# Kernel tuning notes

Hardware: AMD Instinct MI355X
Metric: run time of the kernel (lower is better)

## Reference

```python
import jax, jax.numpy as jnp
import numpy as np

N, E, D, H, L = 10000, 80000, 1024, 8, 2
C = D // H          # 128 per-head channels
NEG = 0.2           # GATv2 default negative_slope


def setup_inputs() -> dict:
    k = jax.random.split(jax.random.key(0), 16)
    s = 0.02
    return {
        "x": jax.random.normal(k[0], (N, D), jnp.float32),
        "edge_index": jax.random.randint(k[1], (2, E), 0, N),
        "edge_attr": jax.random.randint(k[2], (E,), 0, 3),
        "node_types": jax.random.randint(k[3], (N,), 0, 5),
        "node_type_emb": s * jax.random.normal(k[4], (5, D), jnp.float32),
        "edge_type_emb": s * jax.random.normal(k[5], (3, D), jnp.float32),
        "Wl": s * jax.random.normal(k[6], (L, D, D), jnp.float32),
        "bl": jnp.zeros((L, D), jnp.float32),
        "Wr": s * jax.random.normal(k[7], (L, D, D), jnp.float32),
        "br": jnp.zeros((L, D), jnp.float32),
        "We": s * jax.random.normal(k[8], (L, D, D), jnp.float32),
        "att": s * jax.random.normal(k[9], (L, H, C), jnp.float32),
        "conv_bias": jnp.zeros((L, D), jnp.float32),
        "out_W": s * jax.random.normal(k[10], (D, D), jnp.float32),
        "out_b": jnp.zeros((D,), jnp.float32),
    }


def _gatv2(h, src, dst, ee, Wl, bl, Wr, br, We, att, b):
    """PyG GATv2Conv: concat=True, add_self_loops=True (fill_value='mean')."""
    n = h.shape[0]
    xl = (h @ Wl + bl).reshape(n, H, C)   # source transform (lin_l)
    xr = (h @ Wr + br).reshape(n, H, C)   # target transform (lin_r)
    # self loops: edge_attr of a loop = mean of raw incoming edge feats
    cnt = jax.ops.segment_sum(jnp.ones(src.shape, jnp.float32), dst, num_segments=n)
    loop_attr = jax.ops.segment_sum(ee, dst, num_segments=n) / jnp.maximum(cnt, 1.0)[:, None]
    loops = jnp.arange(n)
    s2 = jnp.concatenate([src, loops])
    d2 = jnp.concatenate([dst, loops])
    ea = jnp.concatenate([ee, loop_attr], axis=0)          # [E+N, D]
    ep = (ea @ We).reshape(-1, H, C)                        # lin_edge (no bias)
    e = jax.nn.leaky_relu(xl[s2] + xr[d2] + ep, NEG)        # [E+N, H, C]
    logit = jnp.einsum('ehc,hc->eh', e, att)                # attention logits
    # segment softmax over destination nodes (every node has a self loop)
    m = jax.ops.segment_max(logit, d2, num_segments=n)
    a = jnp.exp(logit - m[d2])
    alpha = a / jax.ops.segment_sum(a, d2, num_segments=n)[d2]
    out = jax.ops.segment_sum(alpha[:, :, None] * xl[s2], d2, num_segments=n)
    return out.reshape(n, D) + b


def reference(x, edge_index, edge_attr, node_types, node_type_emb, edge_type_emb,
              Wl, bl, Wr, br, We, att, conv_bias, out_W, out_b):
    h = x + node_type_emb[node_types]
    ee = edge_type_emb[edge_attr]
    src, dst = edge_index[0], edge_index[1]
    for i in range(L):  # num_layers = 2
        h = h + jax.nn.relu(_gatv2(h, src, dst, ee, Wl[i], bl[i], Wr[i], br[i],
                                   We[i], att[i], conv_bias[i]))
    return h @ out_W + out_b
```

## Files before the change

### kernel.cpp

```cpp
#include <hip/hip_runtime.h>
#include <hip/hip_bf16.h>
#include <stdint.h>

typedef __bf16 bf16_t;
typedef bf16_t bf16x8 __attribute__((ext_vector_type(8)));
typedef bf16_t bf16x4 __attribute__((ext_vector_type(4)));
typedef float f32x4 __attribute__((ext_vector_type(4)));

#define NN 10000
#define EE 80000
#define DD 1024
#define LL 2
#define MPAD 10112
#define NEGS 0.2f

#define GLOAD_LDS16(g, l) \
    __builtin_amdgcn_global_load_lds((__attribute__((address_space(1))) void*)(void*)(g), \
                                     (__attribute__((address_space(3))) void*)(l), 16, 0, 0)

__global__ __launch_bounds__(256)
void preamble(const float* __restrict__ Wl, const float* __restrict__ Wr,
              const float* __restrict__ outW, bf16_t* __restrict__ WT,
              bf16_t* __restrict__ OWT,
              const float* __restrict__ x, const int* __restrict__ ntypes,
              const float* __restrict__ nte, bf16_t* __restrict__ hbuf,
              const float* __restrict__ bl, const float* __restrict__ br,
              const float* __restrict__ outb, float* __restrict__ biasb,
              float* __restrict__ M3L, int* __restrict__ deg3)
{
    __shared__ float tile[64][65];
    int b = blockIdx.x;
    int tid = threadIdx.x;
    if (b < 1280) {
        int z = b >> 8, rem = b & 255;
        int bx = rem & 15, by = rem >> 4;
        const float* src;
        bf16_t* dstp;
        switch (z) {
            case 0: src = Wl;                       dstp = WT;                        break;
            case 1: src = Wr;                       dstp = WT + (size_t)1024*1024;    break;
            case 2: src = Wl + (size_t)1024*1024;   dstp = WT + (size_t)2*1024*1024;  break;
            case 3: src = Wr + (size_t)1024*1024;   dstp = WT + (size_t)3*1024*1024;  break;
            default: src = outW;                    dstp = OWT;                       break;
        }
        int tx = tid & 15, ty = tid >> 4;
#pragma unroll
        for (int p = 0; p < 4; ++p) {
            int r = ty + p*16;
            f32x4 rv = *(const f32x4*)(src + (size_t)(by*64 + r)*1024 + bx*64 + tx*4);
#pragma unroll
            for (int j = 0; j < 4; ++j) tile[r][tx*4 + j] = rv[j];
        }
        __syncthreads();
        int v = tid & 7, u0 = tid >> 3;
#pragma unroll
        for (int p = 0; p < 2; ++p) {
            int u = u0 + p*32;
            bf16x8 ov;
#pragma unroll
            for (int j = 0; j < 8; ++j) ov[j] = (bf16_t)tile[v*8 + j][u];
            *(bf16x8*)(dstp + (size_t)(bx*64 + u)*1024 + by*64 + v*8) = ov;
        }
    } else if (b < 6336) {
        size_t idx = ((size_t)(b - 1280)*256 + tid) * 8;
        if (idx >= (size_t)MPAD*1024) return;
        int n = (int)(idx >> 10);
        int c = (int)(idx & 1023);
        bf16x8 outv;
        if (n < NN) {
            const float* xp = x + (size_t)n*1024 + c;
            int t = ntypes[n];
            const float* ep = nte + (size_t)t*1024 + c;
            f32x4 xa = *(const f32x4*)(xp);
            f32x4 xb = *(const f32x4*)(xp + 4);
            f32x4 ea = *(const f32x4*)(ep);
            f32x4 eb = *(const f32x4*)(ep + 4);
#pragma unroll
            for (int j = 0; j < 4; ++j) {
                outv[j]     = (bf16_t)(xa[j] + ea[j]);
                outv[4 + j] = (bf16_t)(xb[j] + eb[j]);
            }
        } else {
#pragma unroll
            for (int j = 0; j < 8; ++j) outv[j] = (bf16_t)0.f;
        }
        *(bf16x8*)(hbuf + idx) = outv;
    } else if (b < 6356) {
        int i = (b - 6336)*256 + tid;
        if (i < 4096) {
            int l = i >> 11, j = i & 2047;
            biasb[i] = (j < 1024) ? bl[l*1024 + j] : br[l*1024 + j - 1024];
        } else if (i < 5120) {
            biasb[i] = outb[i - 4096];
        }
    } else if (b < 6380) {
        int i = (b - 6356)*256 + tid;
        if (i < LL*3072) M3L[i] = 0.f;
    } else {
        int i = (b - 6380)*256 + tid;
        if (i < 3*NN) deg3[i] = 0;
    }
}

__global__ __launch_bounds__(256)
void compute_m3_all(const float* __restrict__ ete, const float* __restrict__ We,
                    float* __restrict__ M3L)
{
    int l   = blockIdx.x >> 8;
    int bid = blockIdx.x & 255;
    const float* WeL = We + (size_t)l*1024*1024;
    float* M3 = M3L + l*3072;
    int j  = (bid & 3) * 256 + threadIdx.x;
    int k0 = (bid >> 2) * 16;
    float a0 = 0.f, a1 = 0.f, a2 = 0.f;
#pragma unroll
    for (int kk = 0; kk < 16; ++kk) {
        int k = k0 + kk;
        float w = WeL[(size_t)k*1024 + j];
        a0 += ete[k]        * w;
        a1 += ete[1024 + k] * w;
        a2 += ete[2048 + k] * w;
    }
    atomicAdd(&M3[j],        a0);
    atomicAdd(&M3[1024 + j], a1);
    atomicAdd(&M3[2048 + j], a2);
}

__global__ void hist_k(const int* __restrict__ dsts, const int* __restrict__ etype,
                       int* __restrict__ deg3)
{
    int e = blockIdx.x*256 + threadIdx.x;
    if (e < EE) atomicAdd(&deg3[dsts[e]*3 + etype[e]], 1);
}

__global__ __launch_bounds__(1024)
void scan_csr(const int* __restrict__ deg3, int* __restrict__ rp3, int* __restrict__ cursor3)
{
    __shared__ int tot[1024];
    int t = threadIdx.x;
    int base = t * 30;
    int v[30];
    int run = 0;
#pragma unroll
    for (int j = 0; j < 30; ++j) {
        int i = base + j;
        int d = (i < 3*NN) ? deg3[i] : 0;
        run += d;
        v[j] = run;
    }
    tot[t] = run;
    __syncthreads();
    for (int d = 1; d < 1024; d <<= 1) {
        int xv = (t >= d) ? tot[t - d] : 0;
        __syncthreads();
        tot[t] += xv;
        __syncthreads();
    }
    int ex = (t == 0) ? 0 : tot[t - 1];
#pragma unroll
    for (int j = 0; j < 30; ++j) {
        int i = base + j;
        if (i < 3*NN) {
            int incl = ex + v[j];
            rp3[i + 1] = incl;
            if (i + 1 < 3*NN) cursor3[i + 1] = incl;
        }
    }
    if (t == 0) { rp3[0] = 0; cursor3[0] = 0; }
}

__global__ void fill_csr(const int* __restrict__ srcs, const int* __restrict__ dsts,
                         const int* __restrict__ etype, int* __restrict__ cursor3,
                         int* __restrict__ sorted_src)
{
    int e = blockIdx.x*256 + threadIdx.x;
    if (e < EE) {
        int d = dsts[e];
        int t = etype[e];
        int pos = atomicAdd(&cursor3[d*3 + t], 1);
        sorted_src[pos] = srcs[e];
    }
}

template <typename OT>
__global__ __launch_bounds__(256)
void gemm_bt(const bf16_t* __restrict__ A, const bf16_t* __restrict__ BT,
             const float* __restrict__ bias, OT* __restrict__ Cmat,
             int K, int Ntot, int storeM, int mtiles, int ntiles)
{
    __shared__ __align__(16) bf16_t As[128*64];
    __shared__ __align__(16) bf16_t Bs[128*64];
    const int tid  = threadIdx.x;
    const int wave = tid >> 6;
    const int lane = tid & 63;

    const int GROUP_M = 8;
    int pid = blockIdx.x;
    int in_group = GROUP_M * ntiles;
    int gid = pid / in_group;
    int first_m = gid * GROUP_M;
    int gsz = mtiles - first_m; if (gsz > GROUP_M) gsz = GROUP_M;
    int local = pid % in_group;
    const int m0 = (first_m + (local % gsz)) * 128;
    const int n0 = (local / gsz) * 128;

    const int wm = (wave & 1) * 64;
    const int wn = (wave >> 1) * 64;
    const int quad = lane >> 4;
    const int l16  = lane & 15;

    const int srow = lane >> 3;
    const int gcol = ((lane & 7) ^ srow) * 8;

    f32x4 acc[4][4];
    f32x4 zero = {0.f, 0.f, 0.f, 0.f};
#pragma unroll
    for (int i = 0; i < 4; ++i)
#pragma unroll
        for (int j = 0; j < 4; ++j) acc[i][j] = zero;

    const bf16_t* aBase = A  + (size_t)(m0 + wave*8 + srow) * K + gcol;
    const bf16_t* bBase = BT + (size_t)(n0 + wave*8 + srow) * K + gcol;
    bf16_t* asDst = As + wave*512;
    bf16_t* bsDst = Bs + wave*512;

    for (int k0 = 0; k0 < K; k0 += 64) {
#pragma unroll
        for (int j = 0; j < 4; ++j)
            GLOAD_LDS16(aBase + (size_t)(j*32)*K + k0, asDst + j*2048);
#pragma unroll
        for (int j = 0; j < 4; ++j)
            GLOAD_LDS16(bBase + (size_t)(j*32)*K + k0, bsDst + j*2048);
        __syncthreads();
#pragma unroll
        for (int kk = 0; kk < 2; ++kk) {
            bf16x8 af[4], bfr[4];
#pragma unroll
            for (int mi = 0; mi < 4; ++mi) {
                int row = wm + mi*16 + l16;
                int ch  = ((kk*4 + quad) ^ (row & 7)) * 8;
                af[mi] = *(const bf16x8*)(As + row*64 + ch);
            }
#pragma unroll
            for (int ni = 0; ni < 4; ++ni) {
                int row = wn + ni*16 + l16;
                int ch  = ((kk*4 + quad) ^ (row & 7)) * 8;
                bfr[ni] = *(const bf16x8*)(Bs + row*64 + ch);
            }
#pragma unroll
            for (int mi = 0; mi < 4; ++mi)
#pragma unroll
                for (int ni = 0; ni < 4; ++ni)
                    acc[mi][ni] = __builtin_amdgcn_mfma_f32_16x16x32_bf16(af[mi], bfr[ni], acc[mi][ni], 0, 0, 0);
        }
        __syncthreads();
    }

#pragma unroll
    for (int mi = 0; mi < 4; ++mi) {
#pragma unroll
        for (int ni = 0; ni < 4; ++ni) {
            int col = n0 + wn + ni*16 + l16;
            float bv = bias[col];
#pragma unroll
            for (int r = 0; r < 4; ++r) {
                int row = m0 + wm + mi*16 + quad*4 + r;
                if (row < storeM)
                    Cmat[(size_t)row * Ntot + col] = (OT)(acc[mi][ni][r] + bv);
            }
        }
    }
}

__global__ __launch_bounds__(256)
void fused_edge(const int* __restrict__ rp3, const int* __restrict__ ssrc,
                const bf16_t* __restrict__ XLXR,
                const float* __restrict__ M3, const float* __restrict__ attv,
                const float* __restrict__ cbias, bf16_t* __restrict__ hbuf)
{
    int node = blockIdx.x*2 + (threadIdx.x >> 7);
    int q = threadIdx.x & 127;
    int c8 = q * 8;

    int b   = __builtin_amdgcn_readfirstlane(rp3[3*node]);
    int t1g = __builtin_amdgcn_readfirstlane(rp3[3*node + 1]);
    int t2g = __builtin_amdgcn_readfirstlane(rp3[3*node + 2]);
    int en  = __builtin_amdgcn_readfirstlane(rp3[3*node + 3]);

    bf16x8 xlv = *(const bf16x8*)(XLXR + (size_t)node*2048 + c8);
    bf16x8 xrv = *(const bf16x8*)(XLXR + (size_t)node*2048 + 1024 + c8);
    float xr[8], at[8], q0[8], q1[8], q2[8];
#pragma unroll
    for (int j = 0; j < 8; ++j) xr[j] = (float)xrv[j];
    f32x4 a_lo = *(const f32x4*)(attv + c8);
    f32x4 a_hi = *(const f32x4*)(attv + c8 + 4);
#pragma unroll
    for (int j = 0; j < 4; ++j) { at[j] = a_lo[j]; at[4+j] = a_hi[j]; }
#pragma unroll
    for (int j = 0; j < 8; ++j) {
        q0[j] = xr[j] + M3[c8 + j];
        q1[j] = xr[j] + M3[1024 + c8 + j];
        q2[j] = xr[j] + M3[2048 + c8 + j];
    }

    float acc[8] = {0.f, 0.f, 0.f, 0.f, 0.f, 0.f, 0.f, 0.f};
    float den = 0.f;

    auto body = [&](int i, const float (&p)[8]) {
        int s = ssrc[i];
        bf16x8 xs = *(const bf16x8*)(XLXR + (size_t)s*2048 + c8);
        float x[8];
        float part = 0.f;
#pragma unroll
        for (int j = 0; j < 8; ++j) {
            x[j] = (float)xs[j];
            float v = x[j] + p[j];
            v = fmaxf(v, NEGS * v);
            part += v * at[j];
        }
        part += __shfl_xor(part, 1);
        part += __shfl_xor(part, 2);
        part += __shfl_xor(part, 4);
        part += __shfl_xor(part, 8);
        part = fminf(fmaxf(part, -60.f), 60.f);
        float pe = __expf(part);
        den += pe;
#pragma unroll
        for (int j = 0; j < 8; ++j) acc[j] += pe * x[j];
    };

#pragma unroll 2
    for (int i = b; i < t1g; ++i)   body(i, q0);
#pragma unroll 2
    for (int i = t1g; i < t2g; ++i) body(i, q1);
#pragma unroll 2
    for (int i = t2g; i < en; ++i)  body(i, q2);

    float cnt0 = (float)(t1g - b);
    float cnt1 = (float)(t2g - t1g);
    float cnt2 = (float)(en - t2g);
    float degf = cnt0 + cnt1 + cnt2;
    float inv = 1.f / fmaxf(degf, 1.f);
    float w0 = cnt0 * inv, w1 = cnt1 * inv, w2 = cnt2 * inv;
    float sw = w0 + w1 + w2;
    float sx[8];
    float sp = 0.f;
#pragma unroll
    for (int j = 0; j < 8; ++j) {
        sx[j] = (float)xlv[j];
        float u = sx[j] + xr[j]*(1.f - sw) + w0*q0[j] + w1*q1[j] + w2*q2[j];
        u = fmaxf(u, NEGS * u);
        sp += u * at[j];
    }
    sp += __shfl_xor(sp, 1);
    sp += __shfl_xor(sp, 2);
    sp += __shfl_xor(sp, 4);
    sp += __shfl_xor(sp, 8);
    sp = fminf(fmaxf(sp, -60.f), 60.f);
    float ps = __expf(sp);
    den += ps;
#pragma unroll
    for (int j = 0; j < 8; ++j) acc[j] += ps * sx[j];

    float invd = 1.f / den;
    bf16x8 hv = *(const bf16x8*)(hbuf + (size_t)node*1024 + c8);
    bf16x8 outv;
#pragma unroll
    for (int j = 0; j < 8; ++j)
        outv[j] = (bf16_t)((float)hv[j] + fmaxf(acc[j]*invd + cbias[c8 + j], 0.f));
    *(bf16x8*)(hbuf + (size_t)node*1024 + c8) = outv;
}

extern "C" void kernel_launch(void* const* d_in, const int* in_sizes, int n_in,
                              void* d_out, int out_size, void* d_ws, size_t ws_size,
                              hipStream_t stream)
{
    (void)in_sizes; (void)n_in; (void)out_size; (void)ws_size;
    const float* x     = (const float*)d_in[0];
    const int*   eidx  = (const int*)d_in[1];
    const int*   etype = (const int*)d_in[2];
    const int*   ntyp  = (const int*)d_in[3];
    const float* nte   = (const float*)d_in[4];
    const float* ete   = (const float*)d_in[5];
    const float* Wl    = (const float*)d_in[6];
    const float* bl    = (const float*)d_in[7];
    const float* Wr    = (const float*)d_in[8];
    const float* br    = (const float*)d_in[9];
    const float* We    = (const float*)d_in[10];
    const float* attw  = (const float*)d_in[11];
    const float* cbias = (const float*)d_in[12];
    const float* outW  = (const float*)d_in[13];
    const float* outb  = (const float*)d_in[14];
    const int* srcs = eidx;
    const int* dsts = eidx + EE;

    char* wsp = (char*)d_ws;
    size_t off = 0;
    auto carve = [&](size_t bytes) -> void* {
        void* pp = wsp + off;
        off += (bytes + 255) & ~(size_t)255;
        return pp;
    };
    bf16_t* hbuf  = (bf16_t*)carve((size_t)MPAD*1024*2);
    bf16_t* XLXR  = (bf16_t*)carve((size_t)MPAD*2048*2);
    bf16_t* WT    = (bf16_t*)carve((size_t)LL*2048*1024*2);
    bf16_t* OWT   = (bf16_t*)carve((size_t)1024*1024*2);
    float*  M3L   = (float*)carve((size_t)LL*3072*4);
    float*  biasb = (float*)carve(5120*4);
    int* deg3    = (int*)carve((size_t)3*NN*4);
    int* rp3     = (int*)carve((size_t)(3*NN+1)*4);
    int* cursor3 = (int*)carve((size_t)3*NN*4);
    int* ssrc    = (int*)carve((size_t)EE*4);

    preamble<<<6498, 256, 0, stream>>>(Wl, Wr, outW, WT, OWT,
                                       x, ntyp, nte, hbuf,
                                       bl, br, outb, biasb, M3L, deg3);
    compute_m3_all<<<512, 256, 0, stream>>>(ete, We, M3L);
    hist_k<<<(EE + 255)/256, 256, 0, stream>>>(dsts, etype, deg3);
    scan_csr<<<1, 1024, 0, stream>>>(deg3, rp3, cursor3);
    fill_csr<<<(EE + 255)/256, 256, 0, stream>>>(srcs, dsts, etype, cursor3, ssrc);

    for (int l = 0; l < LL; ++l) {
        gemm_bt<bf16_t><<<79*16, 256, 0, stream>>>(hbuf, WT + (size_t)l*2048*1024,
                                                   biasb + l*2048, XLXR,
                                                   1024, 2048, MPAD, 79, 16);
        fused_edge<<<NN/2, 256, 0, stream>>>(rp3, ssrc, XLXR, M3L + l*3072, attw + l*1024,
                                             cbias + l*1024, hbuf);
    }

    gemm_bt<float><<<79*8, 256, 0, stream>>>(hbuf, OWT, biasb + 4096, (float*)d_out,
                                             1024, 1024, NN, 79, 8);
}
```

Measured before the change: 406.9 us.

## Fold M3 and histogram kernels into preamble; prefetch next edge in gather loop

The separate M3 (edge-type embedding times We) and degree-histogram kernels are merged into the preamble. Each of 24 blocks there now computes a full 1024-long dot product per output with no atomics, and deg3 is zeroed with a memset beforehand. In the fused edge kernel, the three per-type loops become one loop that software-prefetches the next source row before computing the current one. This cuts launch count and aims to hide gather latency, but adds a branch per edge and leaves 24 long-running preamble blocks that may lengthen the preamble's tail.

```diff
diff --git a/kernel.cpp b/kernel.cpp
--- a/kernel.cpp
+++ b/kernel.cpp
@@ -26,7 +26,10 @@
               const float* __restrict__ nte, bf16_t* __restrict__ hbuf,
               const float* __restrict__ bl, const float* __restrict__ br,
               const float* __restrict__ outb, float* __restrict__ biasb,
-              float* __restrict__ M3L, int* __restrict__ deg3)
+              const float* __restrict__ ete, const float* __restrict__ We,
+              float* __restrict__ M3L,
+              const int* __restrict__ dsts, const int* __restrict__ etype,
+              int* __restrict__ deg3)
 {
     __shared__ float tile[64][65];
     int b = blockIdx.x;
@@ -94,43 +97,22 @@
             biasb[i] = outb[i - 4096];
         }
     } else if (b < 6380) {
-        int i = (b - 6356)*256 + tid;
-        if (i < LL*3072) M3L[i] = 0.f;
+        int idx = b - 6356;
+        int l  = idx / 12;
+        int rem = idx % 12;
+        int t  = rem >> 2;
+        int j  = (rem & 3) * 256 + tid;
+        const float* WeL = We + (size_t)l*1024*1024 + j;
+        const float* ev  = ete + t*1024;
+        float a = 0.f;
+#pragma unroll 8
+        for (int k = 0; k < 1024; ++k)
+            a += ev[k] * WeL[(size_t)k*1024];
+        M3L[l*3072 + t*1024 + j] = a;
     } else {
-        int i = (b - 6380)*256 + tid;
-        if (i < 3*NN) deg3[i] = 0;
-    }
-}
-
-__global__ __launch_bounds__(256)
-void compute_m3_all(const float* __restrict__ ete, const float* __restrict__ We,
-                    float* __restrict__ M3L)
-{
-    int l   = blockIdx.x >> 8;
-    int bid = blockIdx.x & 255;
-    const float* WeL = We + (size_t)l*1024*1024;
-    float* M3 = M3L + l*3072;
-    int j  = (bid & 3) * 256 + threadIdx.x;
-    int k0 = (bid >> 2) * 16;
-    float a0 = 0.f, a1 = 0.f, a2 = 0.f;
-#pragma unroll
-    for (int kk = 0; kk < 16; ++kk) {
-        int k = k0 + kk;
-        float w = WeL[(size_t)k*1024 + j];
-        a0 += ete[k]        * w;
-        a1 += ete[1024 + k] * w;
-        a2 += ete[2048 + k] * w;
-    }
-    atomicAdd(&M3[j],        a0);
-    atomicAdd(&M3[1024 + j], a1);
-    atomicAdd(&M3[2048 + j], a2);
-}
-
-__global__ void hist_k(const int* __restrict__ dsts, const int* __restrict__ etype,
-                       int* __restrict__ deg3)
-{
-    int e = blockIdx.x*256 + threadIdx.x;
-    if (e < EE) atomicAdd(&deg3[dsts[e]*3 + etype[e]], 1);
+        int e = (b - 6380)*256 + tid;
+        if (e < EE) atomicAdd(&deg3[dsts[e]*3 + etype[e]], 1);
+    }
 }
 
 __global__ __launch_bounds__(1024)
@@ -306,14 +288,18 @@
     float acc[8] = {0.f, 0.f, 0.f, 0.f, 0.f, 0.f, 0.f, 0.f};
     float den = 0.f;
 
-    auto body = [&](int i, const float (&p)[8]) {
-        int s = ssrc[i];
-        bf16x8 xs = *(const bf16x8*)(XLXR + (size_t)s*2048 + c8);
+    bf16x8 xs_cur, xs_next;
+    if (b < en) {
+        int s0 = ssrc[b];
+        xs_cur = *(const bf16x8*)(XLXR + (size_t)s0*2048 + c8);
+    }
+
+    auto compute = [&](const float (&p)[8]) {
         float x[8];
         float part = 0.f;
 #pragma unroll
         for (int j = 0; j < 8; ++j) {
-            x[j] = (float)xs[j];
+            x[j] = (float)xs_cur[j];
             float v = x[j] + p[j];
             v = fmaxf(v, NEGS * v);
             part += v * at[j];
@@ -329,12 +315,16 @@
         for (int j = 0; j < 8; ++j) acc[j] += pe * x[j];
     };
 
-#pragma unroll 2
-    for (int i = b; i < t1g; ++i)   body(i, q0);
-#pragma unroll 2
-    for (int i = t1g; i < t2g; ++i) body(i, q1);
-#pragma unroll 2
-    for (int i = t2g; i < en; ++i)  body(i, q2);
+    for (int i = b; i < en; ++i) {
+        if (i + 1 < en) {
+            int sn = ssrc[i + 1];
+            xs_next = *(const bf16x8*)(XLXR + (size_t)sn*2048 + c8);
+        }
+        if (i < t1g)      compute(q0);
+        else if (i < t2g) compute(q1);
+        else              compute(q2);
+        xs_cur = xs_next;
+    }
 
     float cnt0 = (float)(t1g - b);
     float cnt1 = (float)(t2g - t1g);
@@ -412,11 +402,12 @@
     int* cursor3 = (int*)carve((size_t)3*NN*4);
     int* ssrc    = (int*)carve((size_t)EE*4);
 
-    preamble<<<6498, 256, 0, stream>>>(Wl, Wr, outW, WT, OWT,
+    hipMemsetAsync(deg3, 0, (size_t)3*NN*4, stream);
+    preamble<<<6693, 256, 0, stream>>>(Wl, Wr, outW, WT, OWT,
                                        x, ntyp, nte, hbuf,
-                                       bl, br, outb, biasb, M3L, deg3);
-    compute_m3_all<<<512, 256, 0, stream>>>(ete, We, M3L);
-    hist_k<<<(EE + 255)/256, 256, 0, stream>>>(dsts, etype, deg3);
+                                       bl, br, outb, biasb,
+                                       ete, We, M3L,
+                                       dsts, etype, deg3);
     scan_csr<<<1, 1024, 0, stream>>>(deg3, rp3, cursor3);
     fill_csr<<<(EE + 255)/256, 256, 0, stream>>>(srcs, dsts, etype, cursor3, ssrc);
 
```

After: 476.6 us. 17.1% more time.
